# Kernel optimization log

Hardware: AMD Instinct MI355X
Metric: run time of the kernel (lower is better)

The kernel has to match this reference:

```python
import jax, jax.numpy as jnp
import numpy as np

EPS = 1e-05
DELTA = 2.0


def setup_inputs() -> dict:
    key = jax.random.key(0)
    k1, k2, k3, k4 = jax.random.split(key, 4)
    b, n, d = 8, 2048, 256
    static_node_emb = jax.random.normal(k1, (n, d), dtype=jnp.float32)
    current_node_emb = jax.random.normal(k2, (b, n, d), dtype=jnp.float32)
    prev_node_emb = jax.random.normal(k3, (b, n, d), dtype=jnp.float32)
    # xavier_normal for (d, 1): std = sqrt(2/(d+1))
    threshold_pool = jax.random.normal(k4, (d, 1), dtype=jnp.float32) * np.sqrt(2.0 / (d + 1))
    gamma = jnp.ones((1,), dtype=jnp.float32)
    beta = jnp.zeros((1,), dtype=jnp.float32)
    return {
        'static_node_emb': static_node_emb,
        'current_node_emb': current_node_emb,
        'prev_node_emb': prev_node_emb,
        'threshold_pool': threshold_pool,
        'gamma': gamma,
        'beta': beta,
    }


def reference(static_node_emb, current_node_emb, prev_node_emb, threshold_pool, gamma, beta):
    # graph: [b, n, n]
    graph = jnp.einsum('bnd,bmd->bnm', current_node_emb, prev_node_emb)
    # static mask: relu(S S^T) > 0  -> {0,1} float [n, n]
    static_sim = jnp.einsum('nd,md->nm', static_node_emb, static_node_emb)
    static_mask = (jax.nn.relu(static_sim) > 0).astype(jnp.float32)
    # masked relu + row-normalize (asym_adj)
    masked = jax.nn.relu(graph * static_mask) + 1e-10
    probs = masked / jnp.sum(masked, axis=-1, keepdims=True)
    # threshold: sigmoid(cur @ pool) scaled by diagonal of probs
    threshold = jax.nn.sigmoid(jnp.einsum('bnd,dg->bng', current_node_emb, threshold_pool))
    threshold_baseline = jnp.diagonal(probs, axis1=-2, axis2=-1)[..., None]  # [b, n, 1]
    threshold = threshold_baseline * threshold
    x = probs - threshold  # broadcast [b,n,n] - [b,n,1]
    pos_mask = (x >= 0).astype(jnp.float32)
    neg_mask = 1.0 - pos_mask
    pos_mask = jax.nn.sigmoid(x) * pos_mask
    # InstanceNorm over last two dims (biased variance)
    mean = jnp.mean(pos_mask, axis=(-2, -1), keepdims=True)
    var = jnp.var(pos_mask, axis=(-2, -1), keepdims=True)
    x_norm = (pos_mask - mean) / jnp.sqrt(var + EPS)
    tau_beta = jnp.exp((gamma * x_norm + beta) * DELTA)
    phi = tau_beta * pos_mask + tau_beta * neg_mask
    return phi
```

## Files before the change

kernel.cpp:

```cpp
#include <hip/hip_runtime.h>
#include <math.h>
#include <stdint.h>


__device__ __forceinline__ float mrn(float a, float b) { return __fmul_rn(a, b); }
__device__ __forceinline__ float arn(float a, float b) { return __fadd_rn(a, b); }

#define GBK 16

__global__ __launch_bounds__(256)
void mask_kernel(const float* __restrict__ S, unsigned char* __restrict__ mask,
                 int n, int d) {
  __shared__ float Xk[GBK][132];
  __shared__ float Yk[GBK][132];
  const int t = threadIdx.x, tx = t & 15, ty = t >> 4;
  const int row0 = blockIdx.y * 128, col0 = blockIdx.x * 128;
  const int r = t >> 1, q = t & 1;
  float acc[8][8] = {};
  for (int kc = 0; kc < d; kc += GBK) {
    __syncthreads();
    const float* xp = &S[(size_t)(row0 + r) * d + kc + q * 8];
    float4 v0 = *reinterpret_cast<const float4*>(xp);
    float4 v1 = *reinterpret_cast<const float4*>(xp + 4);
    const float* yp = &S[(size_t)(col0 + r) * d + kc + q * 8];
    float4 u0 = *reinterpret_cast<const float4*>(yp);
    float4 u1 = *reinterpret_cast<const float4*>(yp + 4);
    Xk[q*8+0][r] = v0.x; Xk[q*8+1][r] = v0.y; Xk[q*8+2][r] = v0.z; Xk[q*8+3][r] = v0.w;
    Xk[q*8+4][r] = v1.x; Xk[q*8+5][r] = v1.y; Xk[q*8+6][r] = v1.z; Xk[q*8+7][r] = v1.w;
    Yk[q*8+0][r] = u0.x; Yk[q*8+1][r] = u0.y; Yk[q*8+2][r] = u0.z; Yk[q*8+3][r] = u0.w;
    Yk[q*8+4][r] = u1.x; Yk[q*8+5][r] = u1.y; Yk[q*8+6][r] = u1.z; Yk[q*8+7][r] = u1.w;
    __syncthreads();
#pragma unroll
    for (int k = 0; k < GBK; ++k) {
      float4 a0 = *reinterpret_cast<const float4*>(&Xk[k][ty * 8]);
      float4 a1 = *reinterpret_cast<const float4*>(&Xk[k][ty * 8 + 4]);
      float4 b0 = *reinterpret_cast<const float4*>(&Yk[k][tx * 4]);
      float4 b1 = *reinterpret_cast<const float4*>(&Yk[k][64 + tx * 4]);
      float a[8] = {a0.x, a0.y, a0.z, a0.w, a1.x, a1.y, a1.z, a1.w};
      float b[8] = {b0.x, b0.y, b0.z, b0.w, b1.x, b1.y, b1.z, b1.w};
#pragma unroll
      for (int i2 = 0; i2 < 8; ++i2)
#pragma unroll
        for (int j2 = 0; j2 < 8; ++j2)
          acc[i2][j2] = __builtin_fmaf(a[i2], b[j2], acc[i2][j2]);
    }
  }
#pragma unroll
  for (int i2 = 0; i2 < 8; ++i2) {
    int gi = row0 + ty * 8 + i2;
    unsigned lo = 0, hi = 0;
#pragma unroll
    for (int j2 = 0; j2 < 4; ++j2) {
      lo |= (acc[i2][j2]     > 0.0f ? 1u : 0u) << (8 * j2);
      hi |= (acc[i2][4 + j2] > 0.0f ? 1u : 0u) << (8 * j2);
    }
    *reinterpret_cast<unsigned*>(&mask[(size_t)gi * n + col0 + tx * 4])      = lo;
    *reinterpret_cast<unsigned*>(&mask[(size_t)gi * n + col0 + 64 + tx * 4]) = hi;
  }
}

__global__ __launch_bounds__(256)
void graph_kernel(const float* __restrict__ cur, const float* __restrict__ prev,
                  const unsigned char* __restrict__ mask, float* __restrict__ wout,
                  int n, int d) {
  __shared__ float Xk[GBK][132];
  __shared__ float Yk[GBK][132];
  const int t = threadIdx.x, tx = t & 15, ty = t >> 4;
  const int row0 = blockIdx.y * 128, col0 = blockIdx.x * 128, bz = blockIdx.z;
  const float* X = cur + (size_t)bz * n * d;
  const float* Y = prev + (size_t)bz * n * d;
  const int r = t >> 1, q = t & 1;
  float acc[8][8] = {};
  for (int kc = 0; kc < d; kc += GBK) {
    __syncthreads();
    const float* xp = &X[(size_t)(row0 + r) * d + kc + q * 8];
    float4 v0 = *reinterpret_cast<const float4*>(xp);
    float4 v1 = *reinterpret_cast<const float4*>(xp + 4);
    const float* yp = &Y[(size_t)(col0 + r) * d + kc + q * 8];
    float4 u0 = *reinterpret_cast<const float4*>(yp);
    float4 u1 = *reinterpret_cast<const float4*>(yp + 4);
    Xk[q*8+0][r] = v0.x; Xk[q*8+1][r] = v0.y; Xk[q*8+2][r] = v0.z; Xk[q*8+3][r] = v0.w;
    Xk[q*8+4][r] = v1.x; Xk[q*8+5][r] = v1.y; Xk[q*8+6][r] = v1.z; Xk[q*8+7][r] = v1.w;
    Yk[q*8+0][r] = u0.x; Yk[q*8+1][r] = u0.y; Yk[q*8+2][r] = u0.z; Yk[q*8+3][r] = u0.w;
    Yk[q*8+4][r] = u1.x; Yk[q*8+5][r] = u1.y; Yk[q*8+6][r] = u1.z; Yk[q*8+7][r] = u1.w;
    __syncthreads();
#pragma unroll
    for (int k = 0; k < GBK; ++k) {
      float4 a0 = *reinterpret_cast<const float4*>(&Xk[k][ty * 8]);
      float4 a1 = *reinterpret_cast<const float4*>(&Xk[k][ty * 8 + 4]);
      float4 b0 = *reinterpret_cast<const float4*>(&Yk[k][tx * 4]);
      float4 b1 = *reinterpret_cast<const float4*>(&Yk[k][64 + tx * 4]);
      float a[8] = {a0.x, a0.y, a0.z, a0.w, a1.x, a1.y, a1.z, a1.w};
      float b[8] = {b0.x, b0.y, b0.z, b0.w, b1.x, b1.y, b1.z, b1.w};
#pragma unroll
      for (int i2 = 0; i2 < 8; ++i2)
#pragma unroll
        for (int j2 = 0; j2 < 8; ++j2)
          acc[i2][j2] = __builtin_fmaf(a[i2], b[j2], acc[i2][j2]);
    }
  }
#pragma unroll
  for (int i2 = 0; i2 < 8; ++i2) {
    int gi = row0 + ty * 8 + i2;
    size_t rb = (size_t)bz * n * n + (size_t)gi * n;
    unsigned mlo = *reinterpret_cast<const unsigned*>(&mask[(size_t)gi * n + col0 + tx * 4]);
    unsigned mhi = *reinterpret_cast<const unsigned*>(&mask[(size_t)gi * n + col0 + 64 + tx * 4]);
    float4 o0, o1;
    o0.x = arn(fmaxf(mrn(acc[i2][0], (float)(mlo & 0xff)), 0.0f), 1e-10f);
    o0.y = arn(fmaxf(mrn(acc[i2][1], (float)((mlo >> 8) & 0xff)), 0.0f), 1e-10f);
    o0.z = arn(fmaxf(mrn(acc[i2][2], (float)((mlo >> 16) & 0xff)), 0.0f), 1e-10f);
    o0.w = arn(fmaxf(mrn(acc[i2][3], (float)((mlo >> 24) & 0xff)), 0.0f), 1e-10f);
    o1.x = arn(fmaxf(mrn(acc[i2][4], (float)(mhi & 0xff)), 0.0f), 1e-10f);
    o1.y = arn(fmaxf(mrn(acc[i2][5], (float)((mhi >> 8) & 0xff)), 0.0f), 1e-10f);
    o1.z = arn(fmaxf(mrn(acc[i2][6], (float)((mhi >> 16) & 0xff)), 0.0f), 1e-10f);
    o1.w = arn(fmaxf(mrn(acc[i2][7], (float)((mhi >> 24) & 0xff)), 0.0f), 1e-10f);
    *reinterpret_cast<float4*>(&wout[rb + col0 + tx * 4])      = o0;
    *reinterpret_cast<float4*>(&wout[rb + col0 + 64 + tx * 4]) = o1;
  }
}

__global__ __launch_bounds__(256)
void tz_kernel(const float* __restrict__ cur, const float* __restrict__ pool,
               float* __restrict__ tv, int nrows, int d) {
  int row = blockIdx.x * 256 + threadIdx.x;
  if (row >= nrows) return;
  const float* x = cur + (size_t)row * d;
  float acc = 0.0f;
  for (int k = 0; k < d; ++k) acc = __builtin_fmaf(x[k], pool[k], acc);
  float e = (float)exp(-(double)acc);
  tv[row] = __fdiv_rn(1.0f, arn(1.0f, e));
}

__global__ __launch_bounds__(256)
void rowfuse_kernel(float* __restrict__ wbuf, const float* __restrict__ tv,
                    double* __restrict__ cpart, int n) {
  const int row = blockIdx.x;
  const int t = threadIdx.x;
  float* a = wbuf + (size_t)row * n;
  const int i = row % n;
  const int kleaf = t >> 4, l = t & 15;
  __shared__ float leaf[16];
  __shared__ float sh_rs, sh_thr;
  {
    const float* base = a + kleaf * 128;
    float r0 = base[l],      r1 = base[16 + l],  r2 = base[32 + l],  r3 = base[48 + l];
    float r4 = base[64 + l], r5 = base[80 + l],  r6 = base[96 + l],  r7 = base[112 + l];
    float v = arn(arn(arn(r0, r1), arn(r2, r3)), arn(arn(r4, r5), arn(r6, r7)));
    v = arn(v, __shfl_xor(v, 8));
    v = arn(v, __shfl_xor(v, 4));
    v = arn(v, __shfl_xor(v, 2));
    v = arn(v, __shfl_xor(v, 1));
    if (l == 0) leaf[kleaf] = v;
  }
  __syncthreads();
  if (t == 0) {
    float t1[8], t2[4], t3[2];
#pragma unroll
    for (int k2 = 0; k2 < 8; ++k2) t1[k2] = arn(leaf[2*k2], leaf[2*k2+1]);
#pragma unroll
    for (int k2 = 0; k2 < 4; ++k2) t2[k2] = arn(t1[2*k2], t1[2*k2+1]);
#pragma unroll
    for (int k2 = 0; k2 < 2; ++k2) t3[k2] = arn(t2[2*k2], t2[2*k2+1]);
    float rs = arn(t3[0], t3[1]);
    sh_rs = rs;
    float tb = __fdiv_rn(a[i], rs);
    sh_thr = mrn(tb, tv[row]);
  }
  __syncthreads();
  const float rs = sh_rs, thr = sh_thr;
  double s1 = 0.0, s2 = 0.0;
  for (int off = 0; off < n; off += 1024) {
    float4 wv = *reinterpret_cast<const float4*>(&a[off + t * 4]);
    float p[4];
    float wa[4] = {wv.x, wv.y, wv.z, wv.w};
#pragma unroll
    for (int c = 0; c < 4; ++c) {
      float probs = __fdiv_rn(wa[c], rs);
      float x = __fsub_rn(probs, thr);
      float pv = 0.0f;
      if (x >= 0.0f) pv = __fdiv_rn(1.0f, arn(1.0f, __expf(-x) == __expf(-x) ? expf(-x) : expf(-x)));
      p[c] = pv;
      s1 += (double)pv;
      s2 += (double)pv * (double)pv;
    }
    float4 ov; ov.x = p[0]; ov.y = p[1]; ov.z = p[2]; ov.w = p[3];
    *reinterpret_cast<float4*>(&a[off + t * 4]) = ov;
  }
  __shared__ double sh1[256], sh2[256];
  sh1[t] = s1; sh2[t] = s2;
  __syncthreads();
  for (int s = 128; s > 0; s >>= 1) {
    if (t < s) { sh1[t] += sh1[t + s]; sh2[t] += sh2[t + s]; }
    __syncthreads();
  }
  if (t == 0) {
    cpart[(size_t)row * 2 + 0] = sh1[0];
    cpart[(size_t)row * 2 + 1] = sh2[0];
  }
}

__global__ __launch_bounds__(256)
void stats_kernel(const double* __restrict__ cpart, float* __restrict__ bstats,
                  int nb, double inv_nn) {
  int b = blockIdx.x, t = threadIdx.x;
  double s1 = 0.0, s2 = 0.0;
  for (int c = t; c < nb; c += 256) {
    s1 += cpart[((size_t)b * nb + c) * 2 + 0];
    s2 += cpart[((size_t)b * nb + c) * 2 + 1];
  }
  __shared__ double sh1[256], sh2[256];
  sh1[t] = s1; sh2[t] = s2;
  __syncthreads();
  for (int s = 128; s > 0; s >>= 1) {
    if (t < s) { sh1[t] += sh1[t + s]; sh2[t] += sh2[t + s]; }
    __syncthreads();
  }
  if (t == 0) {
    double mean = sh1[0] * inv_nn;
    double var = sh2[0] * inv_nn - mean * mean;
    bstats[b * 2 + 0] = (float)mean;
    bstats[b * 2 + 1] = (float)(1.0 / sqrt(var + 1e-5));
  }
}

__global__ void phi_kernel(float4* __restrict__ buf, const float* __restrict__ bstats,
                           const float* __restrict__ gamma, const float* __restrict__ beta,
                           size_t total4, int nn4) {
  size_t idx = (size_t)blockIdx.x * blockDim.x + threadIdx.x;
  if (idx >= total4) return;
  int b = (int)(idx / (size_t)nn4);
  float mean = bstats[b * 2 + 0];
  float inv = bstats[b * 2 + 1];
  float ga = gamma[0] * 2.0f;
  float be = beta[0] * 2.0f;
  float4 v = buf[idx];
  float p, xn, tau;
  p = v.x; xn = (p - mean) * inv; tau = expf(ga * xn + be); v.x = tau * (p > 0.0f ? p : 1.0f);
  p = v.y; xn = (p - mean) * inv; tau = expf(ga * xn + be); v.y = tau * (p > 0.0f ? p : 1.0f);
  p = v.z; xn = (p - mean) * inv; tau = expf(ga * xn + be); v.z = tau * (p > 0.0f ? p : 1.0f);
  p = v.w; xn = (p - mean) * inv; tau = expf(ga * xn + be); v.w = tau * (p > 0.0f ? p : 1.0f);
  buf[idx] = v;
}

extern "C" void kernel_launch(void* const* d_in, const int* in_sizes, int n_in,
                              void* d_out, int out_size, void* d_ws, size_t ws_size,
                              hipStream_t stream) {
  const float* S     = (const float*)d_in[0];
  const float* cur   = (const float*)d_in[1];
  const float* prev  = (const float*)d_in[2];
  const float* pool  = (const float*)d_in[3];
  const float* gamma = (const float*)d_in[4];
  const float* beta  = (const float*)d_in[5];
  const int d = in_sizes[3];
  const int n = in_sizes[0] / d;
  const int b = in_sizes[1] / (n * d);
  float* out = (float*)d_out;

  const int nrows = b * n;

  char* ws = (char*)d_ws;
  float* tv = (float*)ws; ws += (size_t)nrows * sizeof(float);
  ws = (char*)(((uintptr_t)ws + 15) & ~(uintptr_t)15);
  double* cpart = (double*)ws; ws += (size_t)nrows * 2 * sizeof(double);
  float* bstats = (float*)ws;  ws += 64;
  unsigned char* mask = (unsigned char*)ws;

  dim3 blk(256);

  hipLaunchKernelGGL(mask_kernel, dim3(n / 128, n / 128), blk, 0, stream, S, mask, n, d);
  hipLaunchKernelGGL(tz_kernel, dim3((nrows + 255) / 256), blk, 0, stream,
                     cur, pool, tv, nrows, d);
  hipLaunchKernelGGL(graph_kernel, dim3(n / 128, n / 128, b), blk, 0, stream,
                     cur, prev, mask, out, n, d);
  hipLaunchKernelGGL(rowfuse_kernel, dim3(nrows), blk, 0, stream, out, tv, cpart, n);
  hipLaunchKernelGGL(stats_kernel, dim3(b), blk, 0, stream,
                     cpart, bstats, n, 1.0 / ((double)n * (double)n));
  size_t total4 = (size_t)b * n * n / 4;
  hipLaunchKernelGGL(phi_kernel, dim3((unsigned)((total4 + 255) / 256)), blk, 0, stream,
                     (float4*)out, bstats, gamma, beta, total4, n * n / 4);
}
```

Baseline: 368.0 us.

## Double-buffer GEMM shared tiles and recompute sigmoid in phi to skip writeback

Both GEMM kernels (mask and graph) now use double-buffered shared-memory tiles with register prefetch of the next K-chunk, so one barrier per iteration replaces two and global loads overlap the FMA loop. The row-statistics kernel no longer writes the sigmoid-masked values back to the output buffer. It only stores the per-row sum and threshold, and the phi kernel recomputes probs, the mask and the sigmoid from the raw masked graph values. This removes a full write pass over the b*n*n buffer but repeats the division and exponential work in phi.

```diff
diff --git a/kernel.cpp b/kernel.cpp
--- a/kernel.cpp
+++ b/kernel.cpp
@@ -11,31 +11,44 @@
 __global__ __launch_bounds__(256)
 void mask_kernel(const float* __restrict__ S, unsigned char* __restrict__ mask,
                  int n, int d) {
-  __shared__ float Xk[GBK][132];
-  __shared__ float Yk[GBK][132];
+  __shared__ float Xk[2][GBK][132];
+  __shared__ float Yk[2][GBK][132];
   const int t = threadIdx.x, tx = t & 15, ty = t >> 4;
   const int row0 = blockIdx.y * 128, col0 = blockIdx.x * 128;
   const int r = t >> 1, q = t & 1;
+  const float* xp = &S[(size_t)(row0 + r) * d + q * 8];
+  const float* yp = &S[(size_t)(col0 + r) * d + q * 8];
   float acc[8][8] = {};
-  for (int kc = 0; kc < d; kc += GBK) {
-    __syncthreads();
-    const float* xp = &S[(size_t)(row0 + r) * d + kc + q * 8];
-    float4 v0 = *reinterpret_cast<const float4*>(xp);
-    float4 v1 = *reinterpret_cast<const float4*>(xp + 4);
-    const float* yp = &S[(size_t)(col0 + r) * d + kc + q * 8];
-    float4 u0 = *reinterpret_cast<const float4*>(yp);
-    float4 u1 = *reinterpret_cast<const float4*>(yp + 4);
-    Xk[q*8+0][r] = v0.x; Xk[q*8+1][r] = v0.y; Xk[q*8+2][r] = v0.z; Xk[q*8+3][r] = v0.w;
-    Xk[q*8+4][r] = v1.x; Xk[q*8+5][r] = v1.y; Xk[q*8+6][r] = v1.z; Xk[q*8+7][r] = v1.w;
-    Yk[q*8+0][r] = u0.x; Yk[q*8+1][r] = u0.y; Yk[q*8+2][r] = u0.z; Yk[q*8+3][r] = u0.w;
-    Yk[q*8+4][r] = u1.x; Yk[q*8+5][r] = u1.y; Yk[q*8+6][r] = u1.z; Yk[q*8+7][r] = u1.w;
-    __syncthreads();
+  float4 v0 = *reinterpret_cast<const float4*>(xp);
+  float4 v1 = *reinterpret_cast<const float4*>(xp + 4);
+  float4 u0 = *reinterpret_cast<const float4*>(yp);
+  float4 u1 = *reinterpret_cast<const float4*>(yp + 4);
+  {
+    float va[8] = {v0.x, v0.y, v0.z, v0.w, v1.x, v1.y, v1.z, v1.w};
+    float ua[8] = {u0.x, u0.y, u0.z, u0.w, u1.x, u1.y, u1.z, u1.w};
+#pragma unroll
+    for (int j = 0; j < 8; ++j) { Xk[0][q*8+j][r] = va[j]; Yk[0][q*8+j][r] = ua[j]; }
+  }
+  __syncthreads();
+  int cur = 0;
+  const int nk = d / GBK;
+  for (int kc = 0; kc < nk; ++kc) {
+    const bool more = (kc + 1 < nk);
+    if (more) {
+      xp += GBK; yp += GBK;
+      v0 = *reinterpret_cast<const float4*>(xp);
+      v1 = *reinterpret_cast<const float4*>(xp + 4);
+      u0 = *reinterpret_cast<const float4*>(yp);
+      u1 = *reinterpret_cast<const float4*>(yp + 4);
+    }
+    const float (*Xc)[132] = Xk[cur];
+    const float (*Yc)[132] = Yk[cur];
 #pragma unroll
     for (int k = 0; k < GBK; ++k) {
-      float4 a0 = *reinterpret_cast<const float4*>(&Xk[k][ty * 8]);
-      float4 a1 = *reinterpret_cast<const float4*>(&Xk[k][ty * 8 + 4]);
-      float4 b0 = *reinterpret_cast<const float4*>(&Yk[k][tx * 4]);
-      float4 b1 = *reinterpret_cast<const float4*>(&Yk[k][64 + tx * 4]);
+      float4 a0 = *reinterpret_cast<const float4*>(&Xc[k][ty * 8]);
+      float4 a1 = *reinterpret_cast<const float4*>(&Xc[k][ty * 8 + 4]);
+      float4 b0 = *reinterpret_cast<const float4*>(&Yc[k][tx * 4]);
+      float4 b1 = *reinterpret_cast<const float4*>(&Yc[k][64 + tx * 4]);
       float a[8] = {a0.x, a0.y, a0.z, a0.w, a1.x, a1.y, a1.z, a1.w};
       float b[8] = {b0.x, b0.y, b0.z, b0.w, b1.x, b1.y, b1.z, b1.w};
 #pragma unroll
@@ -43,6 +56,15 @@
 #pragma unroll
         for (int j2 = 0; j2 < 8; ++j2)
           acc[i2][j2] = __builtin_fmaf(a[i2], b[j2], acc[i2][j2]);
+    }
+    if (more) {
+      float va[8] = {v0.x, v0.y, v0.z, v0.w, v1.x, v1.y, v1.z, v1.w};
+      float ua[8] = {u0.x, u0.y, u0.z, u0.w, u1.x, u1.y, u1.z, u1.w};
+      int nxt = cur ^ 1;
+#pragma unroll
+      for (int j = 0; j < 8; ++j) { Xk[nxt][q*8+j][r] = va[j]; Yk[nxt][q*8+j][r] = ua[j]; }
+      __syncthreads();
+      cur = nxt;
     }
   }
 #pragma unroll
@@ -60,36 +82,49 @@
 }
 
 __global__ __launch_bounds__(256)
-void graph_kernel(const float* __restrict__ cur, const float* __restrict__ prev,
+void graph_kernel(const float* __restrict__ cur_, const float* __restrict__ prev,
                   const unsigned char* __restrict__ mask, float* __restrict__ wout,
                   int n, int d) {
-  __shared__ float Xk[GBK][132];
-  __shared__ float Yk[GBK][132];
+  __shared__ float Xk[2][GBK][132];
+  __shared__ float Yk[2][GBK][132];
   const int t = threadIdx.x, tx = t & 15, ty = t >> 4;
   const int row0 = blockIdx.y * 128, col0 = blockIdx.x * 128, bz = blockIdx.z;
-  const float* X = cur + (size_t)bz * n * d;
+  const float* X = cur_ + (size_t)bz * n * d;
   const float* Y = prev + (size_t)bz * n * d;
   const int r = t >> 1, q = t & 1;
+  const float* xp = &X[(size_t)(row0 + r) * d + q * 8];
+  const float* yp = &Y[(size_t)(col0 + r) * d + q * 8];
   float acc[8][8] = {};
-  for (int kc = 0; kc < d; kc += GBK) {
-    __syncthreads();
-    const float* xp = &X[(size_t)(row0 + r) * d + kc + q * 8];
-    float4 v0 = *reinterpret_cast<const float4*>(xp);
-    float4 v1 = *reinterpret_cast<const float4*>(xp + 4);
-    const float* yp = &Y[(size_t)(col0 + r) * d + kc + q * 8];
-    float4 u0 = *reinterpret_cast<const float4*>(yp);
-    float4 u1 = *reinterpret_cast<const float4*>(yp + 4);
-    Xk[q*8+0][r] = v0.x; Xk[q*8+1][r] = v0.y; Xk[q*8+2][r] = v0.z; Xk[q*8+3][r] = v0.w;
-    Xk[q*8+4][r] = v1.x; Xk[q*8+5][r] = v1.y; Xk[q*8+6][r] = v1.z; Xk[q*8+7][r] = v1.w;
-    Yk[q*8+0][r] = u0.x; Yk[q*8+1][r] = u0.y; Yk[q*8+2][r] = u0.z; Yk[q*8+3][r] = u0.w;
-    Yk[q*8+4][r] = u1.x; Yk[q*8+5][r] = u1.y; Yk[q*8+6][r] = u1.z; Yk[q*8+7][r] = u1.w;
-    __syncthreads();
+  float4 v0 = *reinterpret_cast<const float4*>(xp);
+  float4 v1 = *reinterpret_cast<const float4*>(xp + 4);
+  float4 u0 = *reinterpret_cast<const float4*>(yp);
+  float4 u1 = *reinterpret_cast<const float4*>(yp + 4);
+  {
+    float va[8] = {v0.x, v0.y, v0.z, v0.w, v1.x, v1.y, v1.z, v1.w};
+    float ua[8] = {u0.x, u0.y, u0.z, u0.w, u1.x, u1.y, u1.z, u1.w};
+#pragma unroll
+    for (int j = 0; j < 8; ++j) { Xk[0][q*8+j][r] = va[j]; Yk[0][q*8+j][r] = ua[j]; }
+  }
+  __syncthreads();
+  int cur = 0;
+  const int nk = d / GBK;
+  for (int kc = 0; kc < nk; ++kc) {
+    const bool more = (kc + 1 < nk);
+    if (more) {
+      xp += GBK; yp += GBK;
+      v0 = *reinterpret_cast<const float4*>(xp);
+      v1 = *reinterpret_cast<const float4*>(xp + 4);
+      u0 = *reinterpret_cast<const float4*>(yp);
+      u1 = *reinterpret_cast<const float4*>(yp + 4);
+    }
+    const float (*Xc)[132] = Xk[cur];
+    const float (*Yc)[132] = Yk[cur];
 #pragma unroll
     for (int k = 0; k < GBK; ++k) {
-      float4 a0 = *reinterpret_cast<const float4*>(&Xk[k][ty * 8]);
-      float4 a1 = *reinterpret_cast<const float4*>(&Xk[k][ty * 8 + 4]);
-      float4 b0 = *reinterpret_cast<const float4*>(&Yk[k][tx * 4]);
-      float4 b1 = *reinterpret_cast<const float4*>(&Yk[k][64 + tx * 4]);
+      float4 a0 = *reinterpret_cast<const float4*>(&Xc[k][ty * 8]);
+      float4 a1 = *reinterpret_cast<const float4*>(&Xc[k][ty * 8 + 4]);
+      float4 b0 = *reinterpret_cast<const float4*>(&Yc[k][tx * 4]);
+      float4 b1 = *reinterpret_cast<const float4*>(&Yc[k][64 + tx * 4]);
       float a[8] = {a0.x, a0.y, a0.z, a0.w, a1.x, a1.y, a1.z, a1.w};
       float b[8] = {b0.x, b0.y, b0.z, b0.w, b1.x, b1.y, b1.z, b1.w};
 #pragma unroll
@@ -97,6 +132,15 @@
 #pragma unroll
         for (int j2 = 0; j2 < 8; ++j2)
           acc[i2][j2] = __builtin_fmaf(a[i2], b[j2], acc[i2][j2]);
+    }
+    if (more) {
+      float va[8] = {v0.x, v0.y, v0.z, v0.w, v1.x, v1.y, v1.z, v1.w};
+      float ua[8] = {u0.x, u0.y, u0.z, u0.w, u1.x, u1.y, u1.z, u1.w};
+      int nxt = cur ^ 1;
+#pragma unroll
+      for (int j = 0; j < 8; ++j) { Xk[nxt][q*8+j][r] = va[j]; Yk[nxt][q*8+j][r] = ua[j]; }
+      __syncthreads();
+      cur = nxt;
     }
   }
 #pragma unroll
@@ -132,11 +176,12 @@
 }
 
 __global__ __launch_bounds__(256)
-void rowfuse_kernel(float* __restrict__ wbuf, const float* __restrict__ tv,
+void rowstat_kernel(const float* __restrict__ wbuf, const float* __restrict__ tv,
+                    float* __restrict__ rsv, float* __restrict__ thrv,
                     double* __restrict__ cpart, int n) {
   const int row = blockIdx.x;
   const int t = threadIdx.x;
-  float* a = wbuf + (size_t)row * n;
+  const float* a = wbuf + (size_t)row * n;
   const int i = row % n;
   const int kleaf = t >> 4, l = t & 15;
   __shared__ float leaf[16];
@@ -162,29 +207,27 @@
 #pragma unroll
     for (int k2 = 0; k2 < 2; ++k2) t3[k2] = arn(t2[2*k2], t2[2*k2+1]);
     float rs = arn(t3[0], t3[1]);
-    sh_rs = rs;
     float tb = __fdiv_rn(a[i], rs);
-    sh_thr = mrn(tb, tv[row]);
+    float th = mrn(tb, tv[row]);
+    sh_rs = rs; sh_thr = th;
+    rsv[row] = rs; thrv[row] = th;
   }
   __syncthreads();
   const float rs = sh_rs, thr = sh_thr;
   double s1 = 0.0, s2 = 0.0;
   for (int off = 0; off < n; off += 1024) {
     float4 wv = *reinterpret_cast<const float4*>(&a[off + t * 4]);
-    float p[4];
     float wa[4] = {wv.x, wv.y, wv.z, wv.w};
 #pragma unroll
     for (int c = 0; c < 4; ++c) {
       float probs = __fdiv_rn(wa[c], rs);
       float x = __fsub_rn(probs, thr);
-      float pv = 0.0f;
-      if (x >= 0.0f) pv = __fdiv_rn(1.0f, arn(1.0f, __expf(-x) == __expf(-x) ? expf(-x) : expf(-x)));
-      p[c] = pv;
-      s1 += (double)pv;
-      s2 += (double)pv * (double)pv;
-    }
-    float4 ov; ov.x = p[0]; ov.y = p[1]; ov.z = p[2]; ov.w = p[3];
-    *reinterpret_cast<float4*>(&a[off + t * 4]) = ov;
+      if (x >= 0.0f) {
+        float pv = __fdiv_rn(1.0f, arn(1.0f, expf(-x)));
+        s1 += (double)pv;
+        s2 += (double)pv * (double)pv;
+      }
+    }
   }
   __shared__ double sh1[256], sh2[256];
   sh1[t] = s1; sh2[t] = s2;
@@ -223,22 +266,36 @@
   }
 }
 
-__global__ void phi_kernel(float4* __restrict__ buf, const float* __restrict__ bstats,
-                           const float* __restrict__ gamma, const float* __restrict__ beta,
-                           size_t total4, int nn4) {
+__global__ __launch_bounds__(256)
+void phi_kernel(float4* __restrict__ buf, const float* __restrict__ rsv,
+                const float* __restrict__ thrv, const float* __restrict__ bstats,
+                const float* __restrict__ gamma, const float* __restrict__ beta,
+                size_t total4, int nq, int n) {
   size_t idx = (size_t)blockIdx.x * blockDim.x + threadIdx.x;
   if (idx >= total4) return;
-  int b = (int)(idx / (size_t)nn4);
+  int row = (int)(idx / (size_t)nq);
+  int b = row / n;
+  float rs = rsv[row], thr = thrv[row];
   float mean = bstats[b * 2 + 0];
   float inv = bstats[b * 2 + 1];
   float ga = gamma[0] * 2.0f;
   float be = beta[0] * 2.0f;
   float4 v = buf[idx];
-  float p, xn, tau;
-  p = v.x; xn = (p - mean) * inv; tau = expf(ga * xn + be); v.x = tau * (p > 0.0f ? p : 1.0f);
-  p = v.y; xn = (p - mean) * inv; tau = expf(ga * xn + be); v.y = tau * (p > 0.0f ? p : 1.0f);
-  p = v.z; xn = (p - mean) * inv; tau = expf(ga * xn + be); v.z = tau * (p > 0.0f ? p : 1.0f);
-  p = v.w; xn = (p - mean) * inv; tau = expf(ga * xn + be); v.w = tau * (p > 0.0f ? p : 1.0f);
+  float wa[4] = {v.x, v.y, v.z, v.w};
+  float oa[4];
+#pragma unroll
+  for (int c = 0; c < 4; ++c) {
+    float probs = __fdiv_rn(wa[c], rs);
+    float x = __fsub_rn(probs, thr);
+    float p = 0.0f, m = 1.0f;
+    if (x >= 0.0f) {
+      p = __fdiv_rn(1.0f, arn(1.0f, expf(-x)));
+      m = p;
+    }
+    float xn = (p - mean) * inv;
+    oa[c] = expf(ga * xn + be) * m;
+  }
+  v.x = oa[0]; v.y = oa[1]; v.z = oa[2]; v.w = oa[3];
   buf[idx] = v;
 }
 
@@ -259,7 +316,9 @@
   const int nrows = b * n;
 
   char* ws = (char*)d_ws;
-  float* tv = (float*)ws; ws += (size_t)nrows * sizeof(float);
+  float* tv   = (float*)ws; ws += (size_t)nrows * sizeof(float);
+  float* rsv  = (float*)ws; ws += (size_t)nrows * sizeof(float);
+  float* thrv = (float*)ws; ws += (size_t)nrows * sizeof(float);
   ws = (char*)(((uintptr_t)ws + 15) & ~(uintptr_t)15);
   double* cpart = (double*)ws; ws += (size_t)nrows * 2 * sizeof(double);
   float* bstats = (float*)ws;  ws += 64;
@@ -272,10 +331,11 @@
                      cur, pool, tv, nrows, d);
   hipLaunchKernelGGL(graph_kernel, dim3(n / 128, n / 128, b), blk, 0, stream,
                      cur, prev, mask, out, n, d);
-  hipLaunchKernelGGL(rowfuse_kernel, dim3(nrows), blk, 0, stream, out, tv, cpart, n);
+  hipLaunchKernelGGL(rowstat_kernel, dim3(nrows), blk, 0, stream,
+                     out, tv, rsv, thrv, cpart, n);
   hipLaunchKernelGGL(stats_kernel, dim3(b), blk, 0, stream,
                      cpart, bstats, n, 1.0 / ((double)n * (double)n));
   size_t total4 = (size_t)b * n * n / 4;
   hipLaunchKernelGGL(phi_kernel, dim3((unsigned)((total4 + 255) / 256)), blk, 0, stream,
-                     (float4*)out, bstats, gamma, beta, total4, n * n / 4);
-}
+                     (float4*)out, rsv, thrv, bstats, gamma, beta, total4, n / 4, n);
+}
```

Measured after the change: 452.5 us. 1.23x slower.

## Use packed FMA in GEMMs and recompute sigmoid mask in phi instead of storing

Applied to the files above, without the earlier changes.

The GEMM inner loops now accumulate into 2-wide float vectors with elementwise fma, so the compiler can emit packed FP32 FMA instructions. The row kernel no longer writes the sigmoid mask back to the output buffer. It only stores per-row sums and thresholds, and the phi kernel recomputes probs, the threshold comparison and the sigmoid from the raw graph values. This removes one full write pass over the large b×n×n buffer, at the cost of an extra division and exp per element in phi.

```diff
diff --git a/kernel.cpp b/kernel.cpp
--- a/kernel.cpp
+++ b/kernel.cpp
@@ -2,6 +2,8 @@
 #include <math.h>
 #include <stdint.h>
 
+
+typedef float f32x2 __attribute__((ext_vector_type(2)));
 
 __device__ __forceinline__ float mrn(float a, float b) { return __fmul_rn(a, b); }
 __device__ __forceinline__ float arn(float a, float b) { return __fadd_rn(a, b); }
@@ -16,7 +18,7 @@
   const int t = threadIdx.x, tx = t & 15, ty = t >> 4;
   const int row0 = blockIdx.y * 128, col0 = blockIdx.x * 128;
   const int r = t >> 1, q = t & 1;
-  float acc[8][8] = {};
+  f32x2 acc[8][4] = {};
   for (int kc = 0; kc < d; kc += GBK) {
     __syncthreads();
     const float* xp = &S[(size_t)(row0 + r) * d + kc + q * 8];
@@ -37,40 +39,47 @@
       float4 b0 = *reinterpret_cast<const float4*>(&Yk[k][tx * 4]);
       float4 b1 = *reinterpret_cast<const float4*>(&Yk[k][64 + tx * 4]);
       float a[8] = {a0.x, a0.y, a0.z, a0.w, a1.x, a1.y, a1.z, a1.w};
-      float b[8] = {b0.x, b0.y, b0.z, b0.w, b1.x, b1.y, b1.z, b1.w};
-#pragma unroll
-      for (int i2 = 0; i2 < 8; ++i2)
-#pragma unroll
-        for (int j2 = 0; j2 < 8; ++j2)
-          acc[i2][j2] = __builtin_fmaf(a[i2], b[j2], acc[i2][j2]);
+      f32x2 b2[4];
+      b2[0].x = b0.x; b2[0].y = b0.y; b2[1].x = b0.z; b2[1].y = b0.w;
+      b2[2].x = b1.x; b2[2].y = b1.y; b2[3].x = b1.z; b2[3].y = b1.w;
+#pragma unroll
+      for (int i2 = 0; i2 < 8; ++i2) {
+        f32x2 av; av.x = a[i2]; av.y = a[i2];
+#pragma unroll
+        for (int j = 0; j < 4; ++j)
+          acc[i2][j] = __builtin_elementwise_fma(av, b2[j], acc[i2][j]);
+      }
     }
   }
 #pragma unroll
   for (int i2 = 0; i2 < 8; ++i2) {
     int gi = row0 + ty * 8 + i2;
     unsigned lo = 0, hi = 0;
-#pragma unroll
-    for (int j2 = 0; j2 < 4; ++j2) {
-      lo |= (acc[i2][j2]     > 0.0f ? 1u : 0u) << (8 * j2);
-      hi |= (acc[i2][4 + j2] > 0.0f ? 1u : 0u) << (8 * j2);
-    }
+    lo |= (acc[i2][0].x > 0.0f ? 1u : 0u);
+    lo |= (acc[i2][0].y > 0.0f ? 1u : 0u) << 8;
+    lo |= (acc[i2][1].x > 0.0f ? 1u : 0u) << 16;
+    lo |= (acc[i2][1].y > 0.0f ? 1u : 0u) << 24;
+    hi |= (acc[i2][2].x > 0.0f ? 1u : 0u);
+    hi |= (acc[i2][2].y > 0.0f ? 1u : 0u) << 8;
+    hi |= (acc[i2][3].x > 0.0f ? 1u : 0u) << 16;
+    hi |= (acc[i2][3].y > 0.0f ? 1u : 0u) << 24;
     *reinterpret_cast<unsigned*>(&mask[(size_t)gi * n + col0 + tx * 4])      = lo;
     *reinterpret_cast<unsigned*>(&mask[(size_t)gi * n + col0 + 64 + tx * 4]) = hi;
   }
 }
 
 __global__ __launch_bounds__(256)
-void graph_kernel(const float* __restrict__ cur, const float* __restrict__ prev,
+void graph_kernel(const float* __restrict__ cur_, const float* __restrict__ prev,
                   const unsigned char* __restrict__ mask, float* __restrict__ wout,
                   int n, int d) {
   __shared__ float Xk[GBK][132];
   __shared__ float Yk[GBK][132];
   const int t = threadIdx.x, tx = t & 15, ty = t >> 4;
   const int row0 = blockIdx.y * 128, col0 = blockIdx.x * 128, bz = blockIdx.z;
-  const float* X = cur + (size_t)bz * n * d;
+  const float* X = cur_ + (size_t)bz * n * d;
   const float* Y = prev + (size_t)bz * n * d;
   const int r = t >> 1, q = t & 1;
-  float acc[8][8] = {};
+  f32x2 acc[8][4] = {};
   for (int kc = 0; kc < d; kc += GBK) {
     __syncthreads();
     const float* xp = &X[(size_t)(row0 + r) * d + kc + q * 8];
@@ -91,12 +100,16 @@
       float4 b0 = *reinterpret_cast<const float4*>(&Yk[k][tx * 4]);
       float4 b1 = *reinterpret_cast<const float4*>(&Yk[k][64 + tx * 4]);
       float a[8] = {a0.x, a0.y, a0.z, a0.w, a1.x, a1.y, a1.z, a1.w};
-      float b[8] = {b0.x, b0.y, b0.z, b0.w, b1.x, b1.y, b1.z, b1.w};
-#pragma unroll
-      for (int i2 = 0; i2 < 8; ++i2)
-#pragma unroll
-        for (int j2 = 0; j2 < 8; ++j2)
-          acc[i2][j2] = __builtin_fmaf(a[i2], b[j2], acc[i2][j2]);
+      f32x2 b2[4];
+      b2[0].x = b0.x; b2[0].y = b0.y; b2[1].x = b0.z; b2[1].y = b0.w;
+      b2[2].x = b1.x; b2[2].y = b1.y; b2[3].x = b1.z; b2[3].y = b1.w;
+#pragma unroll
+      for (int i2 = 0; i2 < 8; ++i2) {
+        f32x2 av; av.x = a[i2]; av.y = a[i2];
+#pragma unroll
+        for (int j = 0; j < 4; ++j)
+          acc[i2][j] = __builtin_elementwise_fma(av, b2[j], acc[i2][j]);
+      }
     }
   }
 #pragma unroll
@@ -106,14 +119,14 @@
     unsigned mlo = *reinterpret_cast<const unsigned*>(&mask[(size_t)gi * n + col0 + tx * 4]);
     unsigned mhi = *reinterpret_cast<const unsigned*>(&mask[(size_t)gi * n + col0 + 64 + tx * 4]);
     float4 o0, o1;
-    o0.x = arn(fmaxf(mrn(acc[i2][0], (float)(mlo & 0xff)), 0.0f), 1e-10f);
-    o0.y = arn(fmaxf(mrn(acc[i2][1], (float)((mlo >> 8) & 0xff)), 0.0f), 1e-10f);
-    o0.z = arn(fmaxf(mrn(acc[i2][2], (float)((mlo >> 16) & 0xff)), 0.0f), 1e-10f);
-    o0.w = arn(fmaxf(mrn(acc[i2][3], (float)((mlo >> 24) & 0xff)), 0.0f), 1e-10f);
-    o1.x = arn(fmaxf(mrn(acc[i2][4], (float)(mhi & 0xff)), 0.0f), 1e-10f);
-    o1.y = arn(fmaxf(mrn(acc[i2][5], (float)((mhi >> 8) & 0xff)), 0.0f), 1e-10f);
-    o1.z = arn(fmaxf(mrn(acc[i2][6], (float)((mhi >> 16) & 0xff)), 0.0f), 1e-10f);
-    o1.w = arn(fmaxf(mrn(acc[i2][7], (float)((mhi >> 24) & 0xff)), 0.0f), 1e-10f);
+    o0.x = arn(fmaxf(mrn(acc[i2][0].x, (float)(mlo & 0xff)), 0.0f), 1e-10f);
+    o0.y = arn(fmaxf(mrn(acc[i2][0].y, (float)((mlo >> 8) & 0xff)), 0.0f), 1e-10f);
+    o0.z = arn(fmaxf(mrn(acc[i2][1].x, (float)((mlo >> 16) & 0xff)), 0.0f), 1e-10f);
+    o0.w = arn(fmaxf(mrn(acc[i2][1].y, (float)((mlo >> 24) & 0xff)), 0.0f), 1e-10f);
+    o1.x = arn(fmaxf(mrn(acc[i2][2].x, (float)(mhi & 0xff)), 0.0f), 1e-10f);
+    o1.y = arn(fmaxf(mrn(acc[i2][2].y, (float)((mhi >> 8) & 0xff)), 0.0f), 1e-10f);
+    o1.z = arn(fmaxf(mrn(acc[i2][3].x, (float)((mhi >> 16) & 0xff)), 0.0f), 1e-10f);
+    o1.w = arn(fmaxf(mrn(acc[i2][3].y, (float)((mhi >> 24) & 0xff)), 0.0f), 1e-10f);
     *reinterpret_cast<float4*>(&wout[rb + col0 + tx * 4])      = o0;
     *reinterpret_cast<float4*>(&wout[rb + col0 + 64 + tx * 4]) = o1;
   }
@@ -132,11 +145,12 @@
 }
 
 __global__ __launch_bounds__(256)
-void rowfuse_kernel(float* __restrict__ wbuf, const float* __restrict__ tv,
+void rowstat_kernel(const float* __restrict__ wbuf, const float* __restrict__ tv,
+                    float* __restrict__ rsv, float* __restrict__ thrv,
                     double* __restrict__ cpart, int n) {
   const int row = blockIdx.x;
   const int t = threadIdx.x;
-  float* a = wbuf + (size_t)row * n;
+  const float* a = wbuf + (size_t)row * n;
   const int i = row % n;
   const int kleaf = t >> 4, l = t & 15;
   __shared__ float leaf[16];
@@ -162,29 +176,27 @@
 #pragma unroll
     for (int k2 = 0; k2 < 2; ++k2) t3[k2] = arn(t2[2*k2], t2[2*k2+1]);
     float rs = arn(t3[0], t3[1]);
-    sh_rs = rs;
     float tb = __fdiv_rn(a[i], rs);
-    sh_thr = mrn(tb, tv[row]);
+    float th = mrn(tb, tv[row]);
+    sh_rs = rs; sh_thr = th;
+    rsv[row] = rs; thrv[row] = th;
   }
   __syncthreads();
   const float rs = sh_rs, thr = sh_thr;
   double s1 = 0.0, s2 = 0.0;
   for (int off = 0; off < n; off += 1024) {
     float4 wv = *reinterpret_cast<const float4*>(&a[off + t * 4]);
-    float p[4];
     float wa[4] = {wv.x, wv.y, wv.z, wv.w};
 #pragma unroll
     for (int c = 0; c < 4; ++c) {
       float probs = __fdiv_rn(wa[c], rs);
       float x = __fsub_rn(probs, thr);
-      float pv = 0.0f;
-      if (x >= 0.0f) pv = __fdiv_rn(1.0f, arn(1.0f, __expf(-x) == __expf(-x) ? expf(-x) : expf(-x)));
-      p[c] = pv;
-      s1 += (double)pv;
-      s2 += (double)pv * (double)pv;
+      if (x >= 0.0f) {
+        float pv = __fdiv_rn(1.0f, arn(1.0f, expf(-x)));
+        s1 += (double)pv;
+        s2 += (double)pv * (double)pv;
+      }
     }
-    float4 ov; ov.x = p[0]; ov.y = p[1]; ov.z = p[2]; ov.w = p[3];
-    *reinterpret_cast<float4*>(&a[off + t * 4]) = ov;
   }
   __shared__ double sh1[256], sh2[256];
   sh1[t] = s1; sh2[t] = s2;
@@ -223,22 +235,36 @@
   }
 }
 
-__global__ void phi_kernel(float4* __restrict__ buf, const float* __restrict__ bstats,
-                           const float* __restrict__ gamma, const float* __restrict__ beta,
-                           size_t total4, int nn4) {
+__global__ __launch_bounds__(256)
+void phi_kernel(float4* __restrict__ buf, const float* __restrict__ rsv,
+                const float* __restrict__ thrv, const float* __restrict__ bstats,
+                const float* __restrict__ gamma, const float* __restrict__ beta,
+                size_t total4, int nq, int n) {
   size_t idx = (size_t)blockIdx.x * blockDim.x + threadIdx.x;
   if (idx >= total4) return;
-  int b = (int)(idx / (size_t)nn4);
+  int row = (int)(idx / (size_t)nq);
+  int b = row / n;
+  float rs = rsv[row], thr = thrv[row];
   float mean = bstats[b * 2 + 0];
   float inv = bstats[b * 2 + 1];
   float ga = gamma[0] * 2.0f;
   float be = beta[0] * 2.0f;
   float4 v = buf[idx];
-  float p, xn, tau;
-  p = v.x; xn = (p - mean) * inv; tau = expf(ga * xn + be); v.x = tau * (p > 0.0f ? p : 1.0f);
-  p = v.y; xn = (p - mean) * inv; tau = expf(ga * xn + be); v.y = tau * (p > 0.0f ? p : 1.0f);
-  p = v.z; xn = (p - mean) * inv; tau = expf(ga * xn + be); v.z = tau * (p > 0.0f ? p : 1.0f);
-  p = v.w; xn = (p - mean) * inv; tau = expf(ga * xn + be); v.w = tau * (p > 0.0f ? p : 1.0f);
+  float wa[4] = {v.x, v.y, v.z, v.w};
+  float oa[4];
+#pragma unroll
+  for (int c = 0; c < 4; ++c) {
+    float probs = __fdiv_rn(wa[c], rs);
+    float x = __fsub_rn(probs, thr);
+    float p = 0.0f, m = 1.0f;
+    if (x >= 0.0f) {
+      p = __fdiv_rn(1.0f, arn(1.0f, expf(-x)));
+      m = p;
+    }
+    float xn = (p - mean) * inv;
+    oa[c] = expf(ga * xn + be) * m;
+  }
+  v.x = oa[0]; v.y = oa[1]; v.z = oa[2]; v.w = oa[3];
   buf[idx] = v;
 }
 
@@ -259,7 +285,9 @@
   const int nrows = b * n;
 
   char* ws = (char*)d_ws;
-  float* tv = (float*)ws; ws += (size_t)nrows * sizeof(float);
+  float* tv   = (float*)ws; ws += (size_t)nrows * sizeof(float);
+  float* rsv  = (float*)ws; ws += (size_t)nrows * sizeof(float);
+  float* thrv = (float*)ws; ws += (size_t)nrows * sizeof(float);
   ws = (char*)(((uintptr_t)ws + 15) & ~(uintptr_t)15);
   double* cpart = (double*)ws; ws += (size_t)nrows * 2 * sizeof(double);
   float* bstats = (float*)ws;  ws += 64;
@@ -272,10 +300,11 @@
                      cur, pool, tv, nrows, d);
   hipLaunchKernelGGL(graph_kernel, dim3(n / 128, n / 128, b), blk, 0, stream,
                      cur, prev, mask, out, n, d);
-  hipLaunchKernelGGL(rowfuse_kernel, dim3(nrows), blk, 0, stream, out, tv, cpart, n);
+  hipLaunchKernelGGL(rowstat_kernel, dim3(nrows), blk, 0, stream,
+                     out, tv, rsv, thrv, cpart, n);
   hipLaunchKernelGGL(stats_kernel, dim3(b), blk, 0, stream,
                      cpart, bstats, n, 1.0 / ((double)n * (double)n));
   size_t total4 = (size_t)b * n * n / 4;
   hipLaunchKernelGGL(phi_kernel, dim3((unsigned)((total4 + 255) / 256)), blk, 0, stream,
-                     (float4*)out, bstats, gamma, beta, total4, n * n / 4);
-}
+                     (float4*)out, rsv, thrv, bstats, gamma, beta, total4, n / 4, n);
+}
```

Result: no change. 362.8 us (-1.4%).
